# Kernel tuning notes

Measured on AMD Instinct MI355X. Metric: run time of the kernel, lower is better.

Reference implementation:

```python
import jax, jax.numpy as jnp
import numpy as np

EPS = 1e-7


def _project_to_ball(x, max_norm=0.9):
    # keep points strictly inside the unit Poincare ball
    n = jnp.linalg.norm(x, axis=-1, keepdims=True)
    return x * (max_norm / (1.0 + n))


def _poincare_pairwise_dist(x, y, c=1.0):
    # x: (B, d), y: (L, d) -> (B, L) hyperbolic distances
    x2 = jnp.sum(x * x, axis=-1, keepdims=True)            # (B, 1)
    y2 = jnp.sum(y * y, axis=-1, keepdims=True).T          # (1, L)
    xy = x @ y.T                                           # (B, L) GEMM
    sq = jnp.maximum(x2 + y2 - 2.0 * xy, 0.0)              # ||x - y||^2
    denom = jnp.maximum((1.0 - c * x2) * (1.0 - c * y2), EPS)
    arg = jnp.maximum(1.0 + 2.0 * c * sq / denom, 1.0 + EPS)
    return jnp.arccosh(arg) / jnp.sqrt(c)


def setup_inputs() -> dict:
    key = jax.random.key(0)
    k1, k2 = jax.random.split(key)
    z_hyp = _project_to_ball(jax.random.normal(k1, (4096, 256), dtype=jnp.float32))
    leaf_emb = _project_to_ball(jax.random.normal(k2, (50000, 256), dtype=jnp.float32))
    leaf_node_ids = jnp.arange(50000, dtype=jnp.int32)
    threshold = jnp.ones((), dtype=jnp.float32)
    return {"z_hyp": z_hyp, "leaf_emb": leaf_emb,
            "leaf_node_ids": leaf_node_ids, "threshold": threshold}


def reference(z_hyp, leaf_emb, leaf_node_ids, threshold):
    c = 1.0
    dists = _poincare_pairwise_dist(z_hyp, leaf_emb, c)      # (B, L)
    scores = jnp.min(dists, axis=-1)                          # (B,) OOD score
    is_ood = scores > threshold                               # (B,) bool
    k = min(5, leaf_emb.shape[0])
    # topk smallest distances -> negate and take top_k
    _, topk = jax.lax.top_k(-dists, k)                        # (B, 5)
    topk_ids = leaf_node_ids[topk]                            # (B, 5)
    return scores, is_ood, topk_ids
```

## Files before the change

kernel.cpp:

```cpp
#include <hip/hip_runtime.h>
#include <hip/hip_bf16.h>
#include <float.h>
#include <stdint.h>

#define BATCH 4096
#define NLEAF 50000
#define DIM   256
#define BN    128
#define NTILES 391
#define NGRP  (NTILES * 8)
#define MAXC  128
#define NCHUNK 8
#define GPC   ((NGRP + NCHUNK - 1) / NCHUNK)

typedef _Float16 h8  __attribute__((ext_vector_type(8)));
typedef float    f16v __attribute__((ext_vector_type(16)));

__device__ __forceinline__ float h2f(unsigned short u) {
    return (float)__builtin_bit_cast(_Float16, u);
}

__device__ __forceinline__ void insert5v(float key, float (&k)[5]) {
    if (key < k[4]) {
        if (key < k[3]) { k[4]=k[3];
            if (key < k[2]) { k[3]=k[2];
                if (key < k[1]) { k[2]=k[1];
                    if (key < k[0]) { k[1]=k[0]; k[0]=key; } else k[1]=key;
                } else k[2]=key;
            } else k[3]=key;
        } else k[4]=key;
    }
}

__device__ __forceinline__ bool lexless(float k, int i, float K, int I) {
    return (k < K) || (k == K && i < I);
}
__device__ __forceinline__ void insert5lex(float key, int id, float (&k)[5], int (&ix)[5]) {
    if (lexless(key, id, k[4], ix[4])) {
        if (lexless(key, id, k[3], ix[3])) { k[4]=k[3]; ix[4]=ix[3];
            if (lexless(key, id, k[2], ix[2])) { k[3]=k[2]; ix[3]=ix[2];
                if (lexless(key, id, k[1], ix[1])) { k[2]=k[1]; ix[2]=ix[1];
                    if (lexless(key, id, k[0], ix[0])) { k[1]=k[0]; ix[1]=ix[0]; k[0]=key; ix[0]=id; }
                    else { k[1]=key; ix[1]=id; }
                } else { k[2]=key; ix[2]=id; }
            } else { k[3]=key; ix[3]=id; }
        } else { k[4]=key; ix[4]=id; }
    }
}

__device__ __forceinline__ void gload_lds16(const void* g, void* l) {
    __builtin_amdgcn_global_load_lds(
        (const __attribute__((address_space(1))) uint32_t*)g,
        (__attribute__((address_space(3))) uint32_t*)l, 16, 0, 0);
}

__global__ void norms_cvt_k(const float* __restrict__ z, const float* __restrict__ leaf,
                            float* __restrict__ x2, float* __restrict__ afac,
                            float* __restrict__ y2, float* __restrict__ bfac,
                            unsigned short* __restrict__ zf, unsigned short* __restrict__ lf) {
    int wv = (blockIdx.x * 256 + threadIdx.x) >> 6;
    int l = threadIdx.x & 63;
    if (wv >= BATCH + NLEAF) return;
    bool isz = wv < BATCH;
    const float* row = isz ? z + (size_t)wv * DIM : leaf + (size_t)(wv - BATCH) * DIM;
    float4 v = reinterpret_cast<const float4*>(row)[l];
    _Float16 h0 = (_Float16)v.x, h1 = (_Float16)v.y, h2 = (_Float16)v.z, h3 = (_Float16)v.w;
    ushort4 u;
    u.x = __builtin_bit_cast(unsigned short, h0);
    u.y = __builtin_bit_cast(unsigned short, h1);
    u.z = __builtin_bit_cast(unsigned short, h2);
    u.w = __builtin_bit_cast(unsigned short, h3);
    unsigned short* dst = isz ? zf + (size_t)wv * DIM : lf + (size_t)(wv - BATCH) * DIM;
    reinterpret_cast<ushort4*>(dst)[l] = u;
    float s = v.x*v.x + v.y*v.y + v.z*v.z + v.w*v.w;
#pragma unroll
    for (int off = 32; off > 0; off >>= 1) s += __shfl_down(s, off, 64);
    if (l == 0) {
        if (isz) { x2[wv] = s; afac[wv] = 2.0f / (1.0f - s); }
        else { int j = wv - BATCH; y2[j] = s; bfac[j] = 1.0f / (1.0f - s); }
    }
}

__global__ __launch_bounds__(256, 2) void gemm_min_k(
        const unsigned short* __restrict__ zf, const unsigned short* __restrict__ lf,
        const float* __restrict__ x2, const float* __restrict__ y2,
        const float* __restrict__ bfac, unsigned short* __restrict__ mins) {
    extern __shared__ char sm[];
    float2* ybt = (float2*)(sm + 65536);
    float*  xt  = (float*)(sm + 66560);

    const int t = threadIdx.x;
    const int w = t >> 6, l = t & 63;
    const int wr = w >> 1, wc = w & 1;
    const int l31 = l & 31, lg2 = l >> 5;

    const int bid = blockIdx.x;
    const int xcd = bid & 7, q = bid >> 3;
    const int ntile = xcd * 49 + (q >> 5);
    if (ntile >= NTILES) return;
    const int m0 = (q & 31) * 128;
    const int l0 = ntile * BN;

    if (t < 128) {
        xt[t] = x2[m0 + t];
        int gl = l0 + t;
        bool v = gl < NLEAF;
        float bb = v ? bfac[gl] : 0.0f;
        float yy = v ? y2[gl] : 0.0f;
        ybt[t] = make_float2(bb, v ? yy * bb : 1e30f);
    }

    int srcA[4], srcB[4];
#pragma unroll
    for (int j = 0; j < 4; ++j) {
        int slot = j * 256 + t;
        int row = slot >> 3, sl = slot & 7;
        int swz = sl ^ (row & 7);
        srcA[j] = (m0 + row) * 512 + swz * 16;
        int gl = l0 + row; if (gl > NLEAF - 1) gl = NLEAF - 1;
        srcB[j] = gl * 512 + swz * 16;
    }

    f16v acc[2][2];
#pragma unroll
    for (int i = 0; i < 2; ++i)
#pragma unroll
        for (int j = 0; j < 2; ++j)
#pragma unroll
            for (int r = 0; r < 16; ++r) acc[i][j][r] = 0.0f;

    auto stage = [&](int ks, int bsel) {
        char* dst = sm + bsel * 32768;
        const int kb = ks * 128;
#pragma unroll
        for (int j = 0; j < 4; ++j) {
            gload_lds16((const char*)zf + srcA[j] + kb, dst + (j * 256 + w * 64) * 16);
            gload_lds16((const char*)lf + srcB[j] + kb, dst + 16384 + (j * 256 + w * 64) * 16);
        }
    };

    auto compute = [&](int bsel) {
        const char* Ab = sm + bsel * 32768;
        const char* Bb = Ab + 16384;
#pragma unroll
        for (int kk = 0; kk < 4; ++kk) {
            const int cz = kk * 32 + lg2 * 16;
            h8 za[2], lb[2];
#pragma unroll
            for (int f = 0; f < 2; ++f) {
                int ra = wr * 64 + f * 32 + l31;
                za[f] = *(const h8*)(Ab + ra * 128 + (cz ^ ((ra & 7) << 4)));
                int rb = wc * 64 + f * 32 + l31;
                lb[f] = *(const h8*)(Bb + rb * 128 + (cz ^ ((rb & 7) << 4)));
            }
#pragma unroll
            for (int fi = 0; fi < 2; ++fi)
#pragma unroll
                for (int fj = 0; fj < 2; ++fj)
                    acc[fi][fj] = __builtin_amdgcn_mfma_f32_32x32x16_f16(lb[fj], za[fi], acc[fi][fj], 0, 0, 0);
        }
    };

    stage(0, 0);
    __syncthreads();
#pragma unroll
    for (int ks = 0; ks < 4; ++ks) {
        if (ks < 3) stage(ks + 1, (ks + 1) & 1);
        compute(ks & 1);
        __syncthreads();
    }

    float xv[2] = { xt[wr * 64 + l31], xt[wr * 64 + 32 + l31] };
#pragma unroll
    for (int fi = 0; fi < 2; ++fi)
#pragma unroll
        for (int fj = 0; fj < 2; ++fj)
#pragma unroll
            for (int hi = 0; hi < 2; ++hi) {
                float kx[8];
#pragma unroll
                for (int r8 = 0; r8 < 8; ++r8) {
                    int reg = hi * 8 + r8;
                    int L = wc * 64 + fj * 32 + (r8 & 3) + 8 * (r8 >> 2) + 4 * lg2 + 16 * hi;
                    float2 p = ybt[L];
                    float a = acc[fi][fj][reg];
                    kx[r8] = fmaf(p.x, fmaf(-2.0f, a, xv[fi]), p.y);
                }
                float gm = fminf(fminf(fminf(kx[0], kx[1]), fminf(kx[2], kx[3])),
                                 fminf(fminf(kx[4], kx[5]), fminf(kx[6], kx[7])));
                gm = fminf(gm, __shfl_xor(gm, 32, 64));
                if (lg2 == 0) {
                    int g = ntile * 8 + wc * 4 + fj * 2 + hi;
                    _Float16 hgm = (_Float16)fminf(gm, 60000.0f);
                    mins[(size_t)g * BATCH + m0 + wr * 64 + fi * 32 + l31] =
                        __builtin_bit_cast(unsigned short, hgm);
                }
            }
}

__global__ __launch_bounds__(256) void select1_k(const unsigned short* __restrict__ mins,
                                                 float* __restrict__ part5) {
    __shared__ float sm5[4][64][5];
    const int w = threadIdx.x >> 6, l = threadIdx.x & 63;
    const int row = blockIdx.x * 64 + l;
    const int jb = w * ((GPC + 3) / 4);
    const int je = min(GPC, jb + (GPC + 3) / 4);
    float t5[5] = {FLT_MAX, FLT_MAX, FLT_MAX, FLT_MAX, FLT_MAX};
    int j = jb;
    for (; j + 4 <= je; j += 4) {
        int g = blockIdx.y * GPC + j;
        float a0 = (g     < NGRP) ? h2f(mins[(size_t)g * BATCH + row]) : FLT_MAX;
        float a1 = (g + 1 < NGRP) ? h2f(mins[(size_t)(g + 1) * BATCH + row]) : FLT_MAX;
        float a2 = (g + 2 < NGRP) ? h2f(mins[(size_t)(g + 2) * BATCH + row]) : FLT_MAX;
        float a3 = (g + 3 < NGRP) ? h2f(mins[(size_t)(g + 3) * BATCH + row]) : FLT_MAX;
        float m4 = fminf(fminf(a0, a1), fminf(a2, a3));
        if (m4 < t5[4]) {
            insert5v(a0, t5); insert5v(a1, t5); insert5v(a2, t5); insert5v(a3, t5);
        }
    }
    for (; j < je; ++j) {
        int g = blockIdx.y * GPC + j;
        float a = (g < NGRP) ? h2f(mins[(size_t)g * BATCH + row]) : FLT_MAX;
        insert5v(a, t5);
    }
#pragma unroll
    for (int q = 0; q < 5; ++q) sm5[w][l][q] = t5[q];
    __syncthreads();
    if (w == 0) {
#pragma unroll
        for (int ww = 1; ww < 4; ++ww)
#pragma unroll
            for (int q = 0; q < 5; ++q) insert5v(sm5[ww][l][q], t5);
#pragma unroll
        for (int q = 0; q < 5; ++q)
            part5[((size_t)row * NCHUNK + blockIdx.y) * 5 + q] = t5[q];
    }
}

__global__ void select_merge_k(const float* __restrict__ part5,
                               float* __restrict__ rowthr, int* __restrict__ cnt) {
    int row = blockIdx.x * 256 + threadIdx.x;
    if (row >= BATCH) return;
    float t5[5] = {FLT_MAX, FLT_MAX, FLT_MAX, FLT_MAX, FLT_MAX};
    const float* p = part5 + (size_t)row * NCHUNK * 5;
    for (int s = 0; s < NCHUNK * 5; ++s) insert5v(p[s], t5);
    rowthr[row] = t5[4] + 2e-3f * fabsf(t5[4]) + 1.8e-2f;
    cnt[row] = 0;
}

__global__ __launch_bounds__(256) void select_scan_k(const unsigned short* __restrict__ mins,
                                                     const float* __restrict__ rowthr,
                                                     int* __restrict__ cnt,
                                                     int* __restrict__ cand) {
    const int w = threadIdx.x >> 6, l = threadIdx.x & 63;
    const int row = blockIdx.x * 64 + l;
    const float thr = rowthr[row];
    const int jb = w * ((GPC + 3) / 4);
    const int je = min(GPC, jb + (GPC + 3) / 4);
    for (int j = jb; j < je; ++j) {
        int g = blockIdx.y * GPC + j;
        if (g >= NGRP) break;
        float m = h2f(mins[(size_t)g * BATCH + row]);
        if (m <= thr) {
            int c = atomicAdd(&cnt[row], 1);
            if (c < MAXC) cand[row * MAXC + c] = g;
        }
    }
}

__global__ __launch_bounds__(512) void recheck_k(
        const float* __restrict__ z, const float* __restrict__ leaf,
        const float* __restrict__ x2, const float* __restrict__ y2,
        const float* __restrict__ bfac, const float* __restrict__ afac,
        const int* __restrict__ cnt, const int* __restrict__ cand,
        const int* __restrict__ ids, const float* __restrict__ thr,
        float* __restrict__ out) {
    __shared__ float mk[40];
    __shared__ int   mi[40];
    const int row = blockIdx.x;
    const int t = threadIdx.x, w = t >> 6, l = t & 63;
    float4 zr = *(const float4*)(z + (size_t)row * DIM + l * 4);
    const float x2r = x2[row];
    int nc = cnt[row]; if (nc > MAXC) nc = MAXC;
    float k5[5]; int i5[5];
#pragma unroll
    for (int q = 0; q < 5; ++q) { k5[q] = FLT_MAX; i5[q] = 0x7FFFFFFF; }
    for (int ci = w; ci < nc; ci += 8) {
        int g = cand[row * MAXC + ci];
#pragma unroll 4
        for (int jj = 0; jj < 16; ++jj) {
            int id = g * 16 + jj;
            int idc = (id < NLEAF) ? id : (NLEAF - 1);
            float4 lfv = *(const float4*)(leaf + (size_t)idc * DIM + l * 4);
            float d = zr.x * lfv.x;
            d = fmaf(zr.y, lfv.y, d); d = fmaf(zr.z, lfv.z, d); d = fmaf(zr.w, lfv.w, d);
#pragma unroll
            for (int s = 1; s < 64; s <<= 1) d += __shfl_xor(d, s, 64);
            float sq = fmaxf(x2r + y2[idc] - 2.0f * d, 0.0f);
            float key = (id < NLEAF) ? sq * bfac[idc] : FLT_MAX;
            insert5lex(key, (id < NLEAF) ? id : 0x7FFFFFFF, k5, i5);
        }
    }
    if (l == 0) {
#pragma unroll
        for (int q = 0; q < 5; ++q) { mk[w * 5 + q] = k5[q]; mi[w * 5 + q] = i5[q]; }
    }
    __syncthreads();
    if (t == 0) {
        float fk[5]; int fi[5];
#pragma unroll
        for (int q = 0; q < 5; ++q) { fk[q] = FLT_MAX; fi[q] = 0x7FFFFFFF; }
        for (int s = 0; s < 40; ++s) insert5lex(mk[s], mi[s], fk, fi);
        float u = fk[0] * afac[row];
        u = fmaxf(u, 1e-7f);
        float dd = log1pf(u + sqrtf(u * (u + 2.0f)));
        out[row] = dd;
        out[BATCH + row] = (dd > thr[0]) ? 1.0f : 0.0f;
#pragma unroll
        for (int q = 0; q < 5; ++q)
            out[2 * BATCH + (size_t)row * 5 + q] = (float)ids[fi[q]];
    }
}

extern "C" void kernel_launch(void* const* d_in, const int* in_sizes, int n_in,
                              void* d_out, int out_size, void* d_ws, size_t ws_size,
                              hipStream_t stream) {
    const float* z    = (const float*)d_in[0];
    const float* leaf = (const float*)d_in[1];
    const int*   ids  = (const int*)d_in[2];
    const float* thr  = (const float*)d_in[3];
    float* out = (float*)d_out;

    char* ws = (char*)d_ws;
    float* x2   = (float*)(ws + 0);
    float* afac = (float*)(ws + 16384);
    float* y2   = (float*)(ws + 32768);
    float* bfac = (float*)(ws + 232768);
    unsigned short* zf = (unsigned short*)(ws + 432768);
    unsigned short* lf = (unsigned short*)(ws + 2529920);
    unsigned short* mins = (unsigned short*)(ws + 28129920);
    int* cnt  = (int*)(ws + 79379072);
    int* cand = (int*)(ws + 79395456);
    float* part5  = (float*)(ws + 81492608);
    float* rowthr = (float*)(ws + 82147968);

    norms_cvt_k<<<(BATCH + NLEAF + 3) / 4, 256, 0, stream>>>(z, leaf, x2, afac, y2, bfac, zf, lf);
    gemm_min_k<<<8 * 49 * 32, 256, 67072, stream>>>(zf, lf, x2, y2, bfac, mins);
    select1_k<<<dim3(BATCH / 64, NCHUNK), 256, 0, stream>>>(mins, part5);
    select_merge_k<<<(BATCH + 255) / 256, 256, 0, stream>>>(part5, rowthr, cnt);
    select_scan_k<<<dim3(BATCH / 64, NCHUNK), 256, 0, stream>>>(mins, rowthr, cnt, cand);
    recheck_k<<<BATCH, 512, 0, stream>>>(z, leaf, x2, y2, bfac, afac, cnt, cand, ids, thr, out);
}
```

Baseline: 434.9 us.

## Regroup candidate recheck by leaf group with wave-level top-5 merge

The exact-distance recheck is reorganised around leaf groups instead of batch rows. While scanning, the code now also builds per-group lists of (row, candidate) pairs. A new kernel loads each group's 16 leaf rows into registers once and computes dot products for every row that selected that group, writing keys to a buffer. A final kernel then merges keys per row with a 64-bit packed key/id wave-shuffle top-5 network. A fallback per-row kernel handles rows whose group list overflowed. This cuts repeated leaf loads and full-wave shuffle reductions per candidate, at the cost of extra atomics, a large key buffer that reuses the fp16 scratch area, and an unclamped read of the last partial leaf group.

Result: faster. 386.5 us (-11.1%).

```diff
diff --git a/kernel.cpp b/kernel.cpp
--- a/kernel.cpp
+++ b/kernel.cpp
@@ -10,17 +10,31 @@
 #define NTILES 391
 #define NGRP  (NTILES * 8)
 #define MAXC  128
+#define GCAP  2048
 #define NCHUNK 8
 #define GPC   ((NGRP + NCHUNK - 1) / NCHUNK)
 
 typedef _Float16 h8  __attribute__((ext_vector_type(8)));
 typedef float    f16v __attribute__((ext_vector_type(16)));
+typedef unsigned long long u64;
 
 __device__ __forceinline__ float h2f(unsigned short u) {
     return (float)__builtin_bit_cast(_Float16, u);
 }
 
 __device__ __forceinline__ void insert5v(float key, float (&k)[5]) {
+    if (key < k[4]) {
+        if (key < k[3]) { k[4]=k[3];
+            if (key < k[2]) { k[3]=k[2];
+                if (key < k[1]) { k[2]=k[1];
+                    if (key < k[0]) { k[1]=k[0]; k[0]=key; } else k[1]=key;
+                } else k[2]=key;
+            } else k[3]=key;
+        } else k[4]=key;
+    }
+}
+
+__device__ __forceinline__ void insert5u(u64 key, u64 (&k)[5]) {
     if (key < k[4]) {
         if (key < k[3]) { k[4]=k[3];
             if (key < k[2]) { k[3]=k[2];
@@ -47,6 +61,9 @@
         } else { k[4]=key; ix[4]=id; }
     }
 }
+
+__device__ __forceinline__ u64 umin64(u64 a, u64 b) { return a < b ? a : b; }
+__device__ __forceinline__ u64 umax64(u64 a, u64 b) { return a > b ? a : b; }
 
 __device__ __forceinline__ void gload_lds16(const void* g, void* l) {
     __builtin_amdgcn_global_load_lds(
@@ -238,20 +255,27 @@
 }
 
 __global__ void select_merge_k(const float* __restrict__ part5,
-                               float* __restrict__ rowthr, int* __restrict__ cnt) {
-    int row = blockIdx.x * 256 + threadIdx.x;
-    if (row >= BATCH) return;
+                               float* __restrict__ rowthr, int* __restrict__ cnt,
+                               int* __restrict__ ovf, int* __restrict__ gcnt) {
+    int idx = blockIdx.x * 256 + threadIdx.x;
+    if (idx < NGRP) gcnt[idx] = 0;
+    if (idx >= BATCH) return;
+    int row = idx;
     float t5[5] = {FLT_MAX, FLT_MAX, FLT_MAX, FLT_MAX, FLT_MAX};
     const float* p = part5 + (size_t)row * NCHUNK * 5;
     for (int s = 0; s < NCHUNK * 5; ++s) insert5v(p[s], t5);
     rowthr[row] = t5[4] + 2e-3f * fabsf(t5[4]) + 1.8e-2f;
     cnt[row] = 0;
+    ovf[row] = 0;
 }
 
 __global__ __launch_bounds__(256) void select_scan_k(const unsigned short* __restrict__ mins,
                                                      const float* __restrict__ rowthr,
                                                      int* __restrict__ cnt,
-                                                     int* __restrict__ cand) {
+                                                     int* __restrict__ cand,
+                                                     int* __restrict__ gcnt,
+                                                     unsigned int* __restrict__ glist,
+                                                     int* __restrict__ ovf) {
     const int w = threadIdx.x >> 6, l = threadIdx.x & 63;
     const int row = blockIdx.x * 64 + l;
     const float thr = rowthr[row];
@@ -263,21 +287,120 @@
         float m = h2f(mins[(size_t)g * BATCH + row]);
         if (m <= thr) {
             int c = atomicAdd(&cnt[row], 1);
-            if (c < MAXC) cand[row * MAXC + c] = g;
-        }
-    }
-}
-
-__global__ __launch_bounds__(512) void recheck_k(
+            if (c < MAXC) {
+                cand[row * MAXC + c] = g;
+                int s = atomicAdd(&gcnt[g], 1);
+                if (s < GCAP) glist[(size_t)g * GCAP + s] = ((unsigned)row << 7) | (unsigned)c;
+                else ovf[row] = 1;
+            }
+        }
+    }
+}
+
+__global__ __launch_bounds__(256) void recheck_g_k(
+        const float* __restrict__ z, const float* __restrict__ leaf,
+        const float* __restrict__ x2, const float* __restrict__ y2,
+        const float* __restrict__ bfac,
+        const int* __restrict__ gcnt, const unsigned int* __restrict__ glist,
+        float* __restrict__ keybuf) {
+    const int g = blockIdx.x;
+    int n = gcnt[g];
+    if (n <= 0) return;
+    if (n > GCAP) n = GCAP;
+    const int t = threadIdx.x, w = t >> 6, l = t & 63;
+    const int j = l & 15, q = l >> 4;
+    float lr[64];
+    const float* lrow = leaf + (size_t)(g * 16 + j) * DIM + q * 64;
+#pragma unroll
+    for (int tt = 0; tt < 16; ++tt) {
+        float4 v = *(const float4*)(lrow + tt * 4);
+        lr[tt * 4 + 0] = v.x; lr[tt * 4 + 1] = v.y;
+        lr[tt * 4 + 2] = v.z; lr[tt * 4 + 3] = v.w;
+    }
+    const float yb = y2[g * 16 + j], bb = bfac[g * 16 + j];
+    for (int i = w; i < n; i += 4) {
+        unsigned int pk = glist[(size_t)g * GCAP + i];
+        int row = (int)(pk >> 7), ci = (int)(pk & 127u);
+        const float4* z4 = (const float4*)(z + (size_t)row * DIM) + q * 16;
+        float d = 0.0f;
+#pragma unroll
+        for (int tt = 0; tt < 16; ++tt) {
+            float4 v = z4[tt];
+            d = fmaf(v.x, lr[tt * 4 + 0], d);
+            d = fmaf(v.y, lr[tt * 4 + 1], d);
+            d = fmaf(v.z, lr[tt * 4 + 2], d);
+            d = fmaf(v.w, lr[tt * 4 + 3], d);
+        }
+        d += __shfl_xor(d, 16, 64);
+        d += __shfl_xor(d, 32, 64);
+        if (q == 0) {
+            float sq = fmaxf(x2[row] + yb - 2.0f * d, 0.0f);
+            keybuf[((size_t)row * MAXC + ci) * 16 + j] = sq * bb;
+        }
+    }
+}
+
+__global__ __launch_bounds__(256) void final_k(
+        const float* __restrict__ keybuf, const int* __restrict__ cand,
+        const int* __restrict__ cnt, const int* __restrict__ ovf,
+        const float* __restrict__ afac, const int* __restrict__ ids,
+        const float* __restrict__ thr, float* __restrict__ out) {
+    const int t = threadIdx.x, w = t >> 6, l = t & 63;
+    const int row = blockIdx.x * 4 + w;
+    if (ovf[row]) return;
+    int nc = cnt[row]; if (nc > MAXC) nc = MAXC;
+    u64 t5[5] = {~0ull, ~0ull, ~0ull, ~0ull, ~0ull};
+    const float* kb = keybuf + (size_t)row * MAXC * 16;
+    const int* cr = cand + row * MAXC;
+    for (int idx = l; idx < nc * 16; idx += 64) {
+        int ci = idx >> 4, j = idx & 15;
+        float key = kb[ci * 16 + j];
+        unsigned int id = (unsigned)(cr[ci] * 16 + j);
+        u64 pk = ((u64)__float_as_uint(key) << 32) | (u64)id;
+        insert5u(pk, t5);
+    }
+#pragma unroll
+    for (int s = 1; s < 64; s <<= 1) {
+        u64 o[5];
+#pragma unroll
+        for (int qq = 0; qq < 5; ++qq) o[qq] = __shfl_xor(t5[qq], s, 64);
+        u64 n0 = umin64(t5[0], o[0]);
+        u64 n1 = umin64(umin64(t5[1], o[1]), umax64(t5[0], o[0]));
+        u64 n2 = umin64(umin64(t5[2], o[2]),
+                 umin64(umax64(t5[0], o[1]), umax64(t5[1], o[0])));
+        u64 n3 = umin64(umin64(t5[3], o[3]),
+                 umin64(umax64(t5[0], o[2]),
+                 umin64(umax64(t5[1], o[1]), umax64(t5[2], o[0]))));
+        u64 n4 = umin64(umin64(t5[4], o[4]),
+                 umin64(umin64(umax64(t5[0], o[3]), umax64(t5[1], o[2])),
+                        umin64(umax64(t5[2], o[1]), umax64(t5[3], o[0]))));
+        t5[0]=n0; t5[1]=n1; t5[2]=n2; t5[3]=n3; t5[4]=n4;
+    }
+    if (l == 0) {
+        float k0 = __uint_as_float((unsigned)(t5[0] >> 32));
+        float u = k0 * afac[row];
+        u = fmaxf(u, 1e-7f);
+        float dd = log1pf(u + sqrtf(u * (u + 2.0f)));
+        out[row] = dd;
+        out[BATCH + row] = (dd > thr[0]) ? 1.0f : 0.0f;
+#pragma unroll
+        for (int qq = 0; qq < 5; ++qq)
+            out[2 * BATCH + (size_t)row * 5 + qq] = (float)ids[(unsigned)(t5[qq] & 0xFFFFFFFFull)];
+    }
+}
+
+__global__ __launch_bounds__(256) void recheck_fb_k(
         const float* __restrict__ z, const float* __restrict__ leaf,
         const float* __restrict__ x2, const float* __restrict__ y2,
         const float* __restrict__ bfac, const float* __restrict__ afac,
         const int* __restrict__ cnt, const int* __restrict__ cand,
+        const int* __restrict__ ovf,
         const int* __restrict__ ids, const float* __restrict__ thr,
         float* __restrict__ out) {
-    __shared__ float mk[40];
-    __shared__ int   mi[40];
+    __shared__ float mk[20];
+    __shared__ int   mi[20];
     const int row = blockIdx.x;
+    if (ovf[row] == 0) return;
     const int t = threadIdx.x, w = t >> 6, l = t & 63;
     float4 zr = *(const float4*)(z + (size_t)row * DIM + l * 4);
     const float x2r = x2[row];
@@ -285,20 +408,20 @@
     float k5[5]; int i5[5];
 #pragma unroll
     for (int q = 0; q < 5; ++q) { k5[q] = FLT_MAX; i5[q] = 0x7FFFFFFF; }
-    for (int ci = w; ci < nc; ci += 8) {
+    for (int ci = w; ci < nc; ci += 4) {
         int g = cand[row * MAXC + ci];
-#pragma unroll 4
+#pragma unroll 1
         for (int jj = 0; jj < 16; ++jj) {
             int id = g * 16 + jj;
-            int idc = (id < NLEAF) ? id : (NLEAF - 1);
-            float4 lfv = *(const float4*)(leaf + (size_t)idc * DIM + l * 4);
+            if (id >= NLEAF) break;
+            float4 lfv = *(const float4*)(leaf + (size_t)id * DIM + l * 4);
             float d = zr.x * lfv.x;
             d = fmaf(zr.y, lfv.y, d); d = fmaf(zr.z, lfv.z, d); d = fmaf(zr.w, lfv.w, d);
 #pragma unroll
             for (int s = 1; s < 64; s <<= 1) d += __shfl_xor(d, s, 64);
-            float sq = fmaxf(x2r + y2[idc] - 2.0f * d, 0.0f);
-            float key = (id < NLEAF) ? sq * bfac[idc] : FLT_MAX;
-            insert5lex(key, (id < NLEAF) ? id : 0x7FFFFFFF, k5, i5);
+            float sq = fmaxf(x2r + y2[id] - 2.0f * d, 0.0f);
+            float key = sq * bfac[id];
+            insert5lex(key, id, k5, i5);
         }
     }
     if (l == 0) {
@@ -310,7 +433,7 @@
         float fk[5]; int fi[5];
 #pragma unroll
         for (int q = 0; q < 5; ++q) { fk[q] = FLT_MAX; fi[q] = 0x7FFFFFFF; }
-        for (int s = 0; s < 40; ++s) insert5lex(mk[s], mi[s], fk, fi);
+        for (int s = 0; s < 20; ++s) insert5lex(mk[s], mi[s], fk, fi);
         float u = fk[0] * afac[row];
         u = fmaxf(u, 1e-7f);
         float dd = log1pf(u + sqrtf(u * (u + 2.0f)));
@@ -339,15 +462,21 @@
     unsigned short* zf = (unsigned short*)(ws + 432768);
     unsigned short* lf = (unsigned short*)(ws + 2529920);
     unsigned short* mins = (unsigned short*)(ws + 28129920);
-    int* cnt  = (int*)(ws + 79379072);
-    int* cand = (int*)(ws + 79395456);
-    float* part5  = (float*)(ws + 81492608);
-    float* rowthr = (float*)(ws + 82147968);
+    int* cnt  = (int*)(ws + 53754496);
+    int* ovf  = (int*)(ws + 53770880);
+    int* gcnt = (int*)(ws + 53787264);
+    int* cand = (int*)(ws + 53803648);
+    float* part5  = (float*)(ws + 55900800);
+    float* rowthr = (float*)(ws + 56556160);
+    unsigned int* glist = (unsigned int*)(ws + 56572544);
+    float* keybuf = (float*)(ws + 432768);
 
     norms_cvt_k<<<(BATCH + NLEAF + 3) / 4, 256, 0, stream>>>(z, leaf, x2, afac, y2, bfac, zf, lf);
     gemm_min_k<<<8 * 49 * 32, 256, 67072, stream>>>(zf, lf, x2, y2, bfac, mins);
     select1_k<<<dim3(BATCH / 64, NCHUNK), 256, 0, stream>>>(mins, part5);
-    select_merge_k<<<(BATCH + 255) / 256, 256, 0, stream>>>(part5, rowthr, cnt);
-    select_scan_k<<<dim3(BATCH / 64, NCHUNK), 256, 0, stream>>>(mins, rowthr, cnt, cand);
-    recheck_k<<<BATCH, 512, 0, stream>>>(z, leaf, x2, y2, bfac, afac, cnt, cand, ids, thr, out);
-}
+    select_merge_k<<<16, 256, 0, stream>>>(part5, rowthr, cnt, ovf, gcnt);
+    select_scan_k<<<dim3(BATCH / 64, NCHUNK), 256, 0, stream>>>(mins, rowthr, cnt, cand, gcnt, glist, ovf);
+    recheck_g_k<<<NGRP, 256, 0, stream>>>(z, leaf, x2, y2, bfac, gcnt, glist, keybuf);
+    final_k<<<BATCH / 4, 256, 0, stream>>>(keybuf, cand, cnt, ovf, afac, ids, thr, out);
+    recheck_fb_k<<<BATCH, 256, 0, stream>>>(z, leaf, x2, y2, bfac, afac, cnt, cand, ovf, ids, thr, out);
+}
```
